# Optimization experiments

Measured on AMD Instinct MI355X. Metric: run time of the kernel, lower is better.

## Reference

```python
import jax, jax.numpy as jnp
import numpy as np

B, S, D, H, P = 2, 2048, 512, 8, 10  # batch, seq, d_model, heads, max_relative_position
DH = D // H
SCALE = float(np.sqrt(D))  # module uses sqrt(d_model) in relative branch


def _rel_indices(len_q, len_k, max_rel):
    rq = jnp.arange(len_q)
    rk = jnp.arange(len_k)
    dist = rk[None, :] - rq[:, None]
    return jnp.clip(dist, -max_rel, max_rel) + max_rel  # [len_q, len_k]


def setup_inputs() -> dict:
    key = jax.random.key(0)
    ks = jax.random.split(key, 12)
    init = lambda k, shp, s=0.02: (jax.random.normal(k, shp, dtype=jnp.float32) * s)
    return {
        "q": jax.random.normal(ks[0], (B, S, D), dtype=jnp.float32),
        "k": jax.random.normal(ks[1], (B, S, D), dtype=jnp.float32),
        "v": jax.random.normal(ks[2], (B, S, D), dtype=jnp.float32),
        "mask": jnp.ones((1, 1, S, S), dtype=jnp.int32),  # no-op in original (masked_fill result discarded)
        "Wq": init(ks[3], (D, D)), "bq": init(ks[4], (D,)),
        "Wk": init(ks[5], (D, D)), "bk": init(ks[6], (D,)),
        "Wv": init(ks[7], (D, D)), "bv": init(ks[8], (D,)),
        "W0": init(ks[9], (D, D)), "b0": init(ks[10], (D,)),
        "rel_k_table": init(ks[11], (2 * P + 1, DH), 0.02),
        "rel_v_table": init(jax.random.fold_in(key, 99), (2 * P + 1, DH), 0.02),
    }


def reference(q, k, v, mask, Wq, bq, Wk, bk, Wv, bv, W0, b0, rel_k_table, rel_v_table):
    # Projections (nn.Linear equivalent with weight stored as [in, out])
    query = q @ Wq + bq  # [B,S,D]
    key_ = k @ Wk + bk
    value = v @ Wv + bv

    qh = query.reshape(B, S, H, DH)  # [B,S,H,DH]
    kh = key_.reshape(B, S, H, DH)
    vh = value.reshape(B, S, H, DH)

    idx = _rel_indices(S, S, P)              # [S,S]
    rel_k = rel_k_table[idx]                 # [S,S,DH]
    rel_v = rel_v_table[idx]                 # [S,S,DH]

    normal_scores = jnp.einsum("bqhd,bkhd->bhqk", qh, kh)
    rel_scores = jnp.einsum("bqhd,qkd->bhqk", qh, rel_k)
    # NOTE: original relative branch applies NO softmax; mask is a no-op (masked_fill not in-place)
    scores = (normal_scores + rel_scores) / SCALE  # [B,H,S,S]

    weight1 = jnp.einsum("bhqk,bkhd->bhqd", scores, vh)
    weight2 = jnp.einsum("bhqk,qkd->bhqd", scores, rel_v)
    x = (weight1 + weight2).transpose(0, 2, 1, 3).reshape(B, S, D)
    return x @ W0 + b0
```

## Files before the change

kernel.cpp:

```cpp
#include <hip/hip_runtime.h>
#include <hip/hip_bf16.h>


typedef __attribute__((ext_vector_type(8)))  short  short8;
typedef __attribute__((ext_vector_type(4)))  short  short4v;
typedef __attribute__((ext_vector_type(16))) float  f32x16;
typedef __attribute__((ext_vector_type(8)))  __bf16 bf16x8;

#define DEV static __device__ __forceinline__

constexpr float INV_SCALE = 0.044194173824159216f;

DEV unsigned short f2bs(float f){ __hip_bfloat16 h = __float2bfloat16(f); unsigned short u; __builtin_memcpy(&u,&h,2); return u; }
DEV short f2b(float f){ return (short)f2bs(f); }
DEV float b2f(short s){ unsigned u = ((unsigned)(unsigned short)s)<<16; float f; __builtin_memcpy(&f,&u,4); return f; }
DEV bf16x8 ld8s(const short* p){ return __builtin_bit_cast(bf16x8, *(const short8*)p); }
DEV f32x16 z16(){ f32x16 z;
#pragma unroll
  for (int i=0;i<16;++i) z[i]=0.f;
  return z; }
DEV f32x16 mfma32(bf16x8 a, bf16x8 b, f32x16 c){ return __builtin_amdgcn_mfma_f32_32x32x16_bf16(a,b,c,0,0,0); }

template<bool AF32, bool OUTB16>
DEV void gemm_body(const void* A, const float* W, const float* bias, void* C,
                   int m0, int n0, short* Alds, short* Blds, short* Xt){
  const int tid = threadIdx.x, lane = tid&63, wid = tid>>6, lo5 = lane&31, hi = lane>>5;
  f32x16 acc0 = z16(), acc1 = z16();
  for (int kt=0; kt<8; ++kt){
    const int k0 = kt*64;
    __syncthreads();
    {
      const int rr = tid>>3, c = tid&7;
#pragma unroll
      for (int p=0;p<4;++p){
        int row = p*32 + rr;
        short8 v;
        if (AF32){
          const float* ap = (const float*)A + (size_t)(m0+row)*512 + k0 + c*8;
          float4 x = *(const float4*)ap; float4 y = *(const float4*)(ap+4);
          v = short8{ f2b(x.x),f2b(x.y),f2b(x.z),f2b(x.w), f2b(y.x),f2b(y.y),f2b(y.z),f2b(y.w) };
        } else {
          v = *(const short8*)((const short*)A + (size_t)(m0+row)*512 + k0 + c*8);
        }
        *(short8*)&Alds[row*64 + ((c ^ (row&7))*8)] = v;
      }
      {
        const int r2 = tid>>2, c4 = tid&3;
        const float* wrow = W + (size_t)(k0+r2)*512 + n0 + c4*16;
        float4 f0 = *(const float4*)(wrow);
        float4 f1 = *(const float4*)(wrow+4);
        float4 f2 = *(const float4*)(wrow+8);
        float4 f3 = *(const float4*)(wrow+12);
        float fv[16] = { f0.x,f0.y,f0.z,f0.w, f1.x,f1.y,f1.z,f1.w,
                         f2.x,f2.y,f2.z,f2.w, f3.x,f3.y,f3.z,f3.w };
        const int kc = r2>>3, ko = r2&7;
#pragma unroll
        for (int e=0;e<16;++e){
          const int n = c4*16 + e;
          Blds[n*64 + ((kc ^ (n&7))*8) + ko] = f2b(fv[e]);
        }
      }
    }
    __syncthreads();
#pragma unroll
    for (int da=0; da<4; ++da){
      const int arow = wid*32 + lo5;
      bf16x8 af = ld8s(&Alds[arow*64 + (((2*da+hi) ^ (arow&7))*8)]);
      const int b0r = lo5, b1r = 32+lo5;
      bf16x8 bf0 = ld8s(&Blds[b0r*64 + (((2*da+hi) ^ (b0r&7))*8)]);
      bf16x8 bf1 = ld8s(&Blds[b1r*64 + (((2*da+hi) ^ (b1r&7))*8)]);
      acc0 = mfma32(af, bf0, acc0);
      acc1 = mfma32(af, bf1, acc1);
    }
  }
  const float bv0 = bias[n0 + lo5], bv1 = bias[n0 + 32 + lo5];
#pragma unroll
  for (int r=0;r<16;++r){
    const int m = m0 + wid*32 + (r&3) + 8*(r>>2) + 4*hi;
    const float v0 = acc0[r] + bv0, v1 = acc1[r] + bv1;
    if (OUTB16){
      ((short*)C)[(size_t)m*512 + n0 + lo5]      = f2b(v0);
      ((short*)C)[(size_t)m*512 + n0 + 32 + lo5] = f2b(v1);
    } else {
      ((float*)C)[(size_t)m*512 + n0 + lo5]      = v0;
      ((float*)C)[(size_t)m*512 + n0 + 32 + lo5] = v1;
    }
  }
  if (Xt){
    __syncthreads();
#pragma unroll
    for (int r=0;r<16;++r){
      const int ml = wid*32 + (r&3) + 8*(r>>2) + 4*hi;
      Alds[ml*64 + lo5]      = f2b(acc0[r] + bv0);
      Alds[ml*64 + 32 + lo5] = f2b(acc1[r] + bv1);
    }
    __syncthreads();
    const int dh = tid & 63, chq = tid >> 6;
    short* xrow = Xt + (size_t)dh*2048 + chq*32;
#pragma unroll
    for (int cp=0; cp<4; ++cp){
      short8 t;
#pragma unroll
      for (int e=0;e<8;++e) t[e] = Alds[(chq*32 + cp*8 + e)*64 + dh];
      *(short8*)(xrow + cp*8) = t;
    }
  }
}

struct ProjArgs { const float* A[3]; const float* W[3]; const float* bias[3]; short* C[3]; short* XT[3]; };

__global__ __launch_bounds__(256) void proj_gemm(ProjArgs args){
  __shared__ short Alds[128*64];
  __shared__ short Blds[64*64];
  const int z = blockIdx.z;
  const int m0 = blockIdx.x*128, n0 = blockIdx.y*64;
  short* xt = nullptr;
  if (args.XT[z]){
    const int b = m0>>11, h = n0>>6, s0 = m0&2047;
    xt = args.XT[z] + ((size_t)(b*8+h)*64)*2048 + s0;
  }
  gemm_body<true,true>(args.A[z], args.W[z], args.bias[z], args.C[z],
                       m0, n0, Alds, Blds, xt);
}

__global__ __launch_bounds__(256) void out_gemm(const short* A, const float* W, const float* bias, float* C){
  __shared__ short Alds[128*64];
  __shared__ short Blds[64*64];
  gemm_body<false,false>(A, W, bias, C, blockIdx.x*128, blockIdx.y*64, Alds, Blds, nullptr);
}

__global__ __launch_bounds__(256) void kvpfx_kernel(const short* Kp, const short* Vp,
    const short* Kt, const short* Vt, float* KVpart, float* KP, float* VP){
  __shared__ float shmem[4*64*64];
  const int blk = blockIdx.x, tid = threadIdx.x;

  if (blk < 128){
    const int bh = blk>>3, ch = blk&7;
    const int lane = tid&63, wid = tid>>6, lo5 = lane&31, hi = lane>>5;
    const short* Ktb = Kt + (size_t)bh*64*2048;
    const short* Vtb = Vt + (size_t)bh*64*2048;
    f32x16 a00=z16(), a01=z16(), a10=z16(), a11=z16();
    const int sb = ch*256 + wid*64;
    for (int s = sb; s < sb+64; s += 16){
      bf16x8 ka = ld8s(Ktb + (size_t)lo5*2048 + s + hi*8);
      bf16x8 kb = ld8s(Ktb + (size_t)(32+lo5)*2048 + s + hi*8);
      bf16x8 va = ld8s(Vtb + (size_t)lo5*2048 + s + hi*8);
      bf16x8 vb = ld8s(Vtb + (size_t)(32+lo5)*2048 + s + hi*8);
      a00 = mfma32(ka, va, a00);
      a01 = mfma32(ka, vb, a01);
      a10 = mfma32(kb, va, a10);
      a11 = mfma32(kb, vb, a11);
    }
    float (*red)[64][64] = (float(*)[64][64])shmem;
#pragma unroll
    for (int r=0;r<16;++r){
      int ir = (r&3) + 8*(r>>2) + 4*hi;
      red[wid][ir][lo5]        = a00[r];
      red[wid][ir][32+lo5]     = a01[r];
      red[wid][32+ir][lo5]     = a10[r];
      red[wid][32+ir][32+lo5]  = a11[r];
    }
    __syncthreads();
    float* dst = KVpart + (size_t)(bh*8+ch)*4096;
    for (int e = tid; e < 4096; e += 256){
      int j = e>>6, i = e&63;
      dst[e] = red[0][i][j] + red[1][i][j] + red[2][i][j] + red[3][i][j];
    }
  } else {
    const int idx = blk - 128;
    const int bh = idx>>2, z = (idx>>1)&1, dhalf = idx&1;
    const int b = bh>>3, h = bh&7;
    const short* X = (z ? Vp : Kp) + (size_t)b*2048*512 + h*64 + dhalf*32;
    float* P = (z ? VP : KP) + (size_t)bh*2048*64 + dhalf*32;
    const int dg = tid & 3;
    const int ch = tid >> 2;
    float (*tot)[4][8] = (float(*)[4][8])shmem;

    const short* xp = X + (size_t)(ch*32)*512 + dg*8;
    float acc[8];
#pragma unroll
    for (int j=0;j<8;++j) acc[j]=0.f;
    for (int i=0;i<32;++i){
      short8 v = *(const short8*)(xp + (size_t)i*512);
#pragma unroll
      for (int j=0;j<8;++j) acc[j] += b2f(v[j]);
    }
#pragma unroll
    for (int j=0;j<8;++j) tot[ch][dg][j] = acc[j];
    __syncthreads();

    float run[8];
#pragma unroll
    for (int j=0;j<8;++j) run[j]=0.f;
    for (int cc=0; cc<ch; ++cc){
      float4 a = *(const float4*)&tot[cc][dg][0];
      float4 c4 = *(const float4*)&tot[cc][dg][4];
      run[0]+=a.x; run[1]+=a.y; run[2]+=a.z; run[3]+=a.w;
      run[4]+=c4.x; run[5]+=c4.y; run[6]+=c4.z; run[7]+=c4.w;
    }
    float* pp = P + (size_t)(ch*32)*64 + dg*8;
    for (int i=0;i<32;++i){
      short8 v = *(const short8*)(xp + (size_t)i*512);
#pragma unroll
      for (int j=0;j<8;++j) run[j] += b2f(v[j]);
      float4 o0 = { run[0], run[1], run[2], run[3] };
      float4 o1 = { run[4], run[5], run[6], run[7] };
      *(float4*)(pp + (size_t)i*64)     = o0;
      *(float4*)(pp + (size_t)i*64 + 4) = o1;
    }
  }
}

__global__ __launch_bounds__(256) void attn2_kernel(const short* Qp, const short* Kp,
    const short* Vt, const float* KVpart, const float* KP, const float* VP,
    const float* relk_g, const float* relv_g, short* xb){
  const int qt = blockIdx.x, bh = blockIdx.y;
  const int b = bh>>3, h = bh&7;
  const int tid = threadIdx.x, lane = tid&63, wid = tid>>6, lo5 = lane&31, hi = lane>>5;
  const int q0 = qt*128, qw = q0 + wid*32;

  __shared__ float Rq[128*21];
  __shared__ short CS[128*32];
  __shared__ short RVT[64*32];
  __shared__ short KVl[64*64];

  for (int i=tid; i<2048; i+=256) ((int*)CS)[i] = 0;
  for (int i=tid; i<2048; i+=256){
    int d = i>>5, j = i&31;
    RVT[d*32 + (j ^ ((d&3)<<3))] = (j<21) ? f2b(relv_g[j*64+d]) : (short)0;
  }

  {
    const int j = tid>>2, i0 = (tid&3)*16;
    float acc[16];
#pragma unroll
    for (int t=0;t<16;++t) acc[t]=0.f;
#pragma unroll
    for (int c=0;c<8;++c){
      const float* p = KVpart + (size_t)(bh*8+c)*4096 + j*64 + i0;
#pragma unroll
      for (int t4=0;t4<4;++t4){
        float4 v = *(const float4*)(p + t4*4);
        acc[t4*4+0]+=v.x; acc[t4*4+1]+=v.y; acc[t4*4+2]+=v.z; acc[t4*4+3]+=v.w;
      }
    }
#pragma unroll
    for (int half=0; half<2; ++half){
      short8 o;
#pragma unroll
      for (int e=0;e<8;++e) o[e] = f2b(acc[half*8+e]);
      const int chunk = (i0>>3) + half;
      *(short8*)&KVl[j*64 + ((chunk ^ (j&7))*8)] = o;
    }
  }

  bf16x8 qf[4];
  {
    const short* Qrow = Qp + (size_t)(b*2048 + qw + lo5)*512 + h*64 + hi*8;
#pragma unroll
    for (int da=0;da<4;++da) qf[da] = ld8s(Qrow + da*16);
  }

  {
    f32x16 rq = z16();
    const int jr = lo5 <= 20 ? lo5 : 20;
    const float* rp = relk_g + jr*64 + hi*8;
#pragma unroll
    for (int da=0;da<4;++da){
      const float* p = rp + da*16;
      float4 x = *(const float4*)p; float4 y = *(const float4*)(p+4);
      short8 rb = { f2b(x.x),f2b(x.y),f2b(x.z),f2b(x.w), f2b(y.x),f2b(y.y),f2b(y.z),f2b(y.w) };
      rq = mfma32(qf[da], __builtin_bit_cast(bf16x8, rb), rq);
    }
    if (lo5 <= 20){
#pragma unroll
      for (int r=0;r<16;++r){
        int qoff = (r&3) + 8*(r>>2) + 4*hi;
        Rq[(wid*32 + qoff)*21 + lo5] = rq[r];
      }
    }
  }
  __syncthreads();

  const int qrow = wid*32 + lo5;
  const int qg = q0 + qrow;

  f32x16 w1a = z16(), w1b = z16();

  {
#pragma unroll
    for (int c=0;c<4;++c){
      const int r0i = lo5, r1i = 32+lo5, ck = 2*c+hi;
      bf16x8 b0v = ld8s(&KVl[r0i*64 + ((ck ^ (r0i&7))*8)]);
      bf16x8 b1v = ld8s(&KVl[r1i*64 + ((ck ^ (r1i&7))*8)]);
      w1a = mfma32(qf[c], b0v, w1a);
      w1b = mfma32(qf[c], b1v, w1b);
    }
  }

  {
    const short* Vg = Vt + (size_t)bh*64*2048;
#pragma unroll
    for (int c=0;c<4;++c){
      const int kb = qw - 16 + c*16;
      const int kbse = kb + hi*8;
      const int jb = kbse - (qw + lo5) + 10;
      short8 av;
#pragma unroll
      for (int e=0;e<8;++e){
        int j = jb + e, kk = kbse + e;
        int jc = j < 1 ? 1 : (j > 19 ? 19 : j);
        float rv = Rq[qrow*21 + jc];
        bool ok = (j>=1) && (j<=19) && (kk>=0) && (kk<2048);
        av[e] = ok ? f2b(rv) : (short)0;
      }
      bf16x8 af = __builtin_bit_cast(bf16x8, av);
      const int kc = kb < 0 ? 0 : (kb > 2048-16 ? 2048-16 : kb);
      bf16x8 v0 = ld8s(Vg + (size_t)lo5*2048 + kc + hi*8);
      bf16x8 v1 = ld8s(Vg + (size_t)(32+lo5)*2048 + kc + hi*8);
      w1a = mfma32(af, v0, w1a);
      w1b = mfma32(af, v1, w1b);
    }
  }

  {
    const float* VPb = VP + (size_t)bh*2048*64;
    const float vt0 = VPb[(size_t)2047*64 + lo5];
    const float vt1 = VPb[(size_t)2047*64 + 32 + lo5];
#pragma unroll
    for (int r=0;r<16;++r){
      const int q_r = qw + (r&3) + 8*(r>>2) + 4*hi;
      const int ql = q_r - q0;
      const float r0q  = Rq[ql*21 + 0];
      const float r20q = Rq[ql*21 + 20];
      float p0=0.f, p1=0.f, s0=0.f, s1=0.f;
      if (q_r >= 10){
        const float* pr = VPb + (size_t)(q_r-10)*64;
        p0 = pr[lo5]; p1 = pr[32+lo5];
      }
      if (q_r <= 2037){
        const float* sr = VPb + (size_t)(q_r+9)*64;
        s0 = vt0 - sr[lo5]; s1 = vt1 - sr[32+lo5];
      }
      w1a[r] += r0q*p0 + r20q*s0;
      w1b[r] += r0q*p1 + r20q*s1;
    }
  }

  {
    const short* Kg = Kp + (size_t)b*2048*512 + h*64;
#pragma unroll
    for (int t3=0; t3<3; ++t3){
      const int kb = qw - 32 + t3*32;
      if (kb < 0 || kb >= 2048) continue;
      const short* Krow = Kg + (size_t)(kb + lo5)*512 + hi*8;
      f32x16 acc = z16();
#pragma unroll
      for (int da=0;da<4;++da) acc = mfma32(ld8s(Krow + da*16), qf[da], acc);
#pragma unroll
      for (int r=0;r<16;++r){
        const int krow = kb + (r&3) + 8*(r>>2) + 4*hi;
        const int j = krow - qg + 10;
        if (j >= 1 && j <= 19)
          CS[qrow*32 + (j ^ ((qrow&3)<<3))] = f2b(acc[r] + Rq[qrow*21 + j]);
      }
    }
  }

  {
    const int half = tid >> 7, q_loc = tid & 127;
    const int q_g2 = q0 + q_loc;
    const short* Qr = Qp + (size_t)(b*2048 + q_g2)*512 + h*64;
    const float* KPb = KP + (size_t)bh*2048*64;
    float val = 0.f;
    if (half == 0){
      if (q_g2 >= 10){
        const float* Pr = KPb + (size_t)(q_g2-10)*64;
        float dot = 0.f;
#pragma unroll
        for (int ii=0; ii<8; ++ii){
          short8 qv = *(const short8*)(Qr + ii*8);
          float4 p0 = *(const float4*)(Pr + ii*8);
          float4 p1 = *(const float4*)(Pr + ii*8 + 4);
          dot += b2f(qv[0])*p0.x + b2f(qv[1])*p0.y + b2f(qv[2])*p0.z + b2f(qv[3])*p0.w
               + b2f(qv[4])*p1.x + b2f(qv[5])*p1.y + b2f(qv[6])*p1.z + b2f(qv[7])*p1.w;
        }
        val = dot + (float)(q_g2 - 9) * Rq[q_loc*21 + 0];
      }
      CS[q_loc*32 + (0 ^ ((q_loc&3)<<3))] = f2b(val);
    } else {
      if (q_g2 <= 2037){
        const float* Pt = KPb + (size_t)2047*64;
        const float* Pr = KPb + (size_t)(q_g2+9)*64;
        float dot = 0.f;
#pragma unroll
        for (int ii=0; ii<8; ++ii){
          short8 qv = *(const short8*)(Qr + ii*8);
          float4 p0 = *(const float4*)(Pr + ii*8);
          float4 t0 = *(const float4*)(Pt + ii*8);
          float4 p1 = *(const float4*)(Pr + ii*8 + 4);
          float4 t1 = *(const float4*)(Pt + ii*8 + 4);
          dot += b2f(qv[0])*(t0.x-p0.x) + b2f(qv[1])*(t0.y-p0.y)
               + b2f(qv[2])*(t0.z-p0.z) + b2f(qv[3])*(t0.w-p0.w)
               + b2f(qv[4])*(t1.x-p1.x) + b2f(qv[5])*(t1.y-p1.y)
               + b2f(qv[6])*(t1.z-p1.z) + b2f(qv[7])*(t1.w-p1.w);
        }
        val = dot + (float)(2038 - q_g2) * Rq[q_loc*21 + 20];
      }
      CS[q_loc*32 + (20 ^ ((q_loc&3)<<3))] = f2b(val);
    }
  }
  __syncthreads();

  f32x16 w2a = z16(), w2b = z16();
#pragma unroll
  for (int c2=0;c2<2;++c2){
    const int arow = wid*32 + lo5;
    bf16x8 cf  = ld8s(&CS[arow*32 + ((16*c2 + 8*hi) ^ ((arow&3)<<3))]);
    const int d0 = lo5, d1 = 32 + lo5;
    bf16x8 rv0 = ld8s(&RVT[d0*32 + ((16*c2 + 8*hi) ^ ((d0&3)<<3))]);
    bf16x8 rv1 = ld8s(&RVT[d1*32 + ((16*c2 + 8*hi) ^ ((d1&3)<<3))]);
    w2a = mfma32(cf, rv0, w2a);
    w2b = mfma32(cf, rv1, w2b);
  }

#pragma unroll
  for (int r=0;r<16;++r){
    const int q_r = qw + (r&3) + 8*(r>>2) + 4*hi;
    const size_t o = ((size_t)b*2048 + q_r)*512 + h*64;
    xb[o + lo5]      = f2b((w1a[r] + w2a[r]) * INV_SCALE);
    xb[o + 32 + lo5] = f2b((w1b[r] + w2b[r]) * INV_SCALE);
  }
}

extern "C" void kernel_launch(void* const* d_in, const int* in_sizes, int n_in,
                              void* d_out, int out_size, void* d_ws, size_t ws_size,
                              hipStream_t stream) {
  (void)in_sizes; (void)n_in; (void)out_size; (void)ws_size;
  const float* q    = (const float*)d_in[0];
  const float* k    = (const float*)d_in[1];
  const float* v    = (const float*)d_in[2];
  const float* Wq   = (const float*)d_in[4];
  const float* bq   = (const float*)d_in[5];
  const float* Wk   = (const float*)d_in[6];
  const float* bk   = (const float*)d_in[7];
  const float* Wv   = (const float*)d_in[8];
  const float* bv   = (const float*)d_in[9];
  const float* W0   = (const float*)d_in[10];
  const float* b0   = (const float*)d_in[11];
  const float* relk = (const float*)d_in[12];
  const float* relv = (const float*)d_in[13];
  float* out = (float*)d_out;
  char* ws = (char*)d_ws;

  short* Qp  = (short*)(ws + ((size_t) 2<<20));
  short* Kp  = (short*)(ws + ((size_t) 6<<20));
  short* Vp  = (short*)(ws + ((size_t)10<<20));
  short* Vt  = (short*)(ws + ((size_t)14<<20));
  short* Kt  = (short*)(ws + ((size_t)18<<20));
  float* KVpart = (float*)(ws + ((size_t)22<<20));
  float* KP  = (float*)(ws + ((size_t)24<<20));
  float* VP  = (float*)(ws + ((size_t)32<<20));
  short* xb  = (short*)(ws + ((size_t)40<<20));

  ProjArgs pa = { {q, k, v}, {Wq, Wk, Wv}, {bq, bk, bv}, {Qp, Kp, Vp},
                  {nullptr, Kt, Vt} };
  proj_gemm<<<dim3(32,8,3), 256, 0, stream>>>(pa);

  kvpfx_kernel<<<192, 256, 0, stream>>>(Kp, Vp, Kt, Vt, KVpart, KP, VP);

  attn2_kernel<<<dim3(16,16), 256, 0, stream>>>(Qp, Kp, Vt, KVpart, KP, VP, relk, relv, xb);

  out_gemm<<<dim3(32,8), 256, 0, stream>>>(xb, W0, b0, out);
}
```

Before: 81.42 us.

## Split attention blocks into 64-query tiles with waves divided over output columns

The attention kernel now handles 64 queries per block instead of 128, and its four waves form a 2x2 grid: two row groups of 32 queries, each split into two 32-wide halves of the head dimension. This doubles the grid to 512 blocks, halves the accumulator registers per wave, and adds a launch-bounds hint for two blocks per CU, aiming at better occupancy and CU coverage. The cost is that the per-block setup (KV partial reduction, RVT table build) is repeated twice as often, and the Q fragment and relative-key work are duplicated across the column waves.

```diff
diff --git a/kernel.cpp b/kernel.cpp
--- a/kernel.cpp
+++ b/kernel.cpp
@@ -211,20 +211,21 @@
   }
 }
 
-__global__ __launch_bounds__(256) void attn2_kernel(const short* Qp, const short* Kp,
+__global__ __launch_bounds__(256,2) void attn2_kernel(const short* Qp, const short* Kp,
     const short* Vt, const float* KVpart, const float* KP, const float* VP,
     const float* relk_g, const float* relv_g, short* xb){
   const int qt = blockIdx.x, bh = blockIdx.y;
   const int b = bh>>3, h = bh&7;
   const int tid = threadIdx.x, lane = tid&63, wid = tid>>6, lo5 = lane&31, hi = lane>>5;
-  const int q0 = qt*128, qw = q0 + wid*32;
-
-  __shared__ float Rq[128*21];
-  __shared__ short CS[128*32];
+  const int rw = wid&1, cw = wid>>1;
+  const int q0 = qt*64, qw = q0 + rw*32;
+
+  __shared__ float Rq[64*21];
+  __shared__ short CS[64*32];
   __shared__ short RVT[64*32];
   __shared__ short KVl[64*64];
 
-  for (int i=tid; i<2048; i+=256) ((int*)CS)[i] = 0;
+  for (int i=tid; i<1024; i+=256) ((int*)CS)[i] = 0;
   for (int i=tid; i<2048; i+=256){
     int d = i>>5, j = i&31;
     RVT[d*32 + (j ^ ((d&3)<<3))] = (j<21) ? f2b(relv_g[j*64+d]) : (short)0;
@@ -261,7 +262,7 @@
     for (int da=0;da<4;++da) qf[da] = ld8s(Qrow + da*16);
   }
 
-  {
+  if (cw == 0){
     f32x16 rq = z16();
     const int jr = lo5 <= 20 ? lo5 : 20;
     const float* rp = relk_g + jr*64 + hi*8;
@@ -276,25 +277,24 @@
 #pragma unroll
       for (int r=0;r<16;++r){
         int qoff = (r&3) + 8*(r>>2) + 4*hi;
-        Rq[(wid*32 + qoff)*21 + lo5] = rq[r];
+        Rq[(rw*32 + qoff)*21 + lo5] = rq[r];
       }
     }
   }
   __syncthreads();
 
-  const int qrow = wid*32 + lo5;
+  const int qrow = rw*32 + lo5;
   const int qg = q0 + qrow;
-
-  f32x16 w1a = z16(), w1b = z16();
+  const int dcol = cw*32 + lo5;
+
+  f32x16 w1 = z16();
 
   {
 #pragma unroll
     for (int c=0;c<4;++c){
-      const int r0i = lo5, r1i = 32+lo5, ck = 2*c+hi;
-      bf16x8 b0v = ld8s(&KVl[r0i*64 + ((ck ^ (r0i&7))*8)]);
-      bf16x8 b1v = ld8s(&KVl[r1i*64 + ((ck ^ (r1i&7))*8)]);
-      w1a = mfma32(qf[c], b0v, w1a);
-      w1b = mfma32(qf[c], b1v, w1b);
+      const int ck = 2*c+hi;
+      bf16x8 bv = ld8s(&KVl[dcol*64 + ((ck ^ (dcol&7))*8)]);
+      w1 = mfma32(qf[c], bv, w1);
     }
   }
 
@@ -316,41 +316,31 @@
       }
       bf16x8 af = __builtin_bit_cast(bf16x8, av);
       const int kc = kb < 0 ? 0 : (kb > 2048-16 ? 2048-16 : kb);
-      bf16x8 v0 = ld8s(Vg + (size_t)lo5*2048 + kc + hi*8);
-      bf16x8 v1 = ld8s(Vg + (size_t)(32+lo5)*2048 + kc + hi*8);
-      w1a = mfma32(af, v0, w1a);
-      w1b = mfma32(af, v1, w1b);
+      bf16x8 v0 = ld8s(Vg + (size_t)dcol*2048 + kc + hi*8);
+      w1 = mfma32(af, v0, w1);
     }
   }
 
   {
     const float* VPb = VP + (size_t)bh*2048*64;
-    const float vt0 = VPb[(size_t)2047*64 + lo5];
-    const float vt1 = VPb[(size_t)2047*64 + 32 + lo5];
+    const float vt0 = VPb[(size_t)2047*64 + dcol];
 #pragma unroll
     for (int r=0;r<16;++r){
       const int q_r = qw + (r&3) + 8*(r>>2) + 4*hi;
       const int ql = q_r - q0;
       const float r0q  = Rq[ql*21 + 0];
       const float r20q = Rq[ql*21 + 20];
-      float p0=0.f, p1=0.f, s0=0.f, s1=0.f;
-      if (q_r >= 10){
-        const float* pr = VPb + (size_t)(q_r-10)*64;
-        p0 = pr[lo5]; p1 = pr[32+lo5];
-      }
-      if (q_r <= 2037){
-        const float* sr = VPb + (size_t)(q_r+9)*64;
-        s0 = vt0 - sr[lo5]; s1 = vt1 - sr[32+lo5];
-      }
-      w1a[r] += r0q*p0 + r20q*s0;
-      w1b[r] += r0q*p1 + r20q*s1;
+      float p0=0.f, s0=0.f;
+      if (q_r >= 10)   p0 = VPb[(size_t)(q_r-10)*64 + dcol];
+      if (q_r <= 2037) s0 = vt0 - VPb[(size_t)(q_r+9)*64 + dcol];
+      w1[r] += r0q*p0 + r20q*s0;
     }
   }
 
   {
     const short* Kg = Kp + (size_t)b*2048*512 + h*64;
-#pragma unroll
-    for (int t3=0; t3<3; ++t3){
+    const int t3lo = cw ? 2 : 0, t3hi = cw ? 3 : 2;
+    for (int t3=t3lo; t3<t3hi; ++t3){
       const int kb = qw - 32 + t3*32;
       if (kb < 0 || kb >= 2048) continue;
       const short* Krow = Kg + (size_t)(kb + lo5)*512 + hi*8;
@@ -368,12 +358,12 @@
   }
 
   {
-    const int half = tid >> 7, q_loc = tid & 127;
+    const int sel = tid >> 6, q_loc = tid & 63;
     const int q_g2 = q0 + q_loc;
     const short* Qr = Qp + (size_t)(b*2048 + q_g2)*512 + h*64;
     const float* KPb = KP + (size_t)bh*2048*64;
-    float val = 0.f;
-    if (half == 0){
+    if (sel == 0){
+      float val = 0.f;
       if (q_g2 >= 10){
         const float* Pr = KPb + (size_t)(q_g2-10)*64;
         float dot = 0.f;
@@ -388,7 +378,8 @@
         val = dot + (float)(q_g2 - 9) * Rq[q_loc*21 + 0];
       }
       CS[q_loc*32 + (0 ^ ((q_loc&3)<<3))] = f2b(val);
-    } else {
+    } else if (sel == 1){
+      float val = 0.f;
       if (q_g2 <= 2037){
         const float* Pt = KPb + (size_t)2047*64;
         const float* Pr = KPb + (size_t)(q_g2+9)*64;
@@ -412,24 +403,19 @@
   }
   __syncthreads();
 
-  f32x16 w2a = z16(), w2b = z16();
+  f32x16 w2 = z16();
 #pragma unroll
   for (int c2=0;c2<2;++c2){
-    const int arow = wid*32 + lo5;
-    bf16x8 cf  = ld8s(&CS[arow*32 + ((16*c2 + 8*hi) ^ ((arow&3)<<3))]);
-    const int d0 = lo5, d1 = 32 + lo5;
-    bf16x8 rv0 = ld8s(&RVT[d0*32 + ((16*c2 + 8*hi) ^ ((d0&3)<<3))]);
-    bf16x8 rv1 = ld8s(&RVT[d1*32 + ((16*c2 + 8*hi) ^ ((d1&3)<<3))]);
-    w2a = mfma32(cf, rv0, w2a);
-    w2b = mfma32(cf, rv1, w2b);
+    bf16x8 cf = ld8s(&CS[qrow*32 + ((16*c2 + 8*hi) ^ ((qrow&3)<<3))]);
+    bf16x8 rv = ld8s(&RVT[dcol*32 + ((16*c2 + 8*hi) ^ ((dcol&3)<<3))]);
+    w2 = mfma32(cf, rv, w2);
   }
 
 #pragma unroll
   for (int r=0;r<16;++r){
     const int q_r = qw + (r&3) + 8*(r>>2) + 4*hi;
-    const size_t o = ((size_t)b*2048 + q_r)*512 + h*64;
-    xb[o + lo5]      = f2b((w1a[r] + w2a[r]) * INV_SCALE);
-    xb[o + 32 + lo5] = f2b((w1b[r] + w2b[r]) * INV_SCALE);
+    const size_t o = ((size_t)b*2048 + q_r)*512 + h*64 + dcol;
+    xb[o] = f2b((w1[r] + w2[r]) * INV_SCALE);
   }
 }
 
@@ -469,7 +455,7 @@
 
   kvpfx_kernel<<<192, 256, 0, stream>>>(Kp, Vp, Kt, Vt, KVpart, KP, VP);
 
-  attn2_kernel<<<dim3(16,16), 256, 0, stream>>>(Qp, Kp, Vt, KVpart, KP, VP, relk, relv, xb);
+  attn2_kernel<<<dim3(32,16), 256, 0, stream>>>(Qp, Kp, Vt, KVpart, KP, VP, relk, relv, xb);
 
   out_gemm<<<dim3(32,8), 256, 0, stream>>>(xb, W0, b0, out);
 }
```

Measured after the change: 83.42 us. 1.02x slower.
